# Kernel tuning notes

Measured on AMD Instinct MI355X. Metric: run time of the kernel, lower is better.

## Reference

```python
import jax, jax.numpy as jnp
import numpy as np
import math


def setup_inputs() -> dict:
    key = jax.random.key(0)
    ks = jax.random.split(key, 7)
    d_input, d_state, d_output = 256, 256, 256
    B_, S_ = 8, 4096
    x = jax.random.normal(ks[0], (B_, S_, d_input), dtype=jnp.float32)
    log_lambda_real = jax.random.normal(ks[1], (d_state,), dtype=jnp.float32)
    lambda_imag = jax.random.normal(ks[2], (d_state,), dtype=jnp.float32)
    dt = jnp.clip(0.01 + jax.random.normal(ks[3], (d_state,), dtype=jnp.float32) * 0.01, 0.005, 0.1)
    log_dt = jnp.log(dt)
    B = jax.random.normal(ks[4], (d_state, d_input), dtype=jnp.float32) / d_state ** 0.5
    C_real = jax.random.normal(ks[5], (d_output, d_state), dtype=jnp.float32) / d_state ** 0.5
    C_imag = jax.random.normal(ks[6], (d_output, d_state), dtype=jnp.float32) / d_state ** 0.5
    return {"x": x, "log_lambda_real": log_lambda_real, "lambda_imag": lambda_imag,
            "log_dt": log_dt, "B": B, "C_real": C_real, "C_imag": C_imag}


def reference(x, log_lambda_real, lambda_imag, log_dt, B, C_real, C_imag):
    batch, seq_len, _ = x.shape
    # continuous-time poles and step sizes
    Lambda = -jnp.exp(log_lambda_real) + 1j * lambda_imag            # [N] complex
    dt = jnp.clip(jnp.exp(log_dt), 0.005, 0.1)                       # [N]
    # bilinear discretization
    denom = 1.0 - 0.5 * dt * Lambda                                  # [N] complex
    A_bar = (1.0 + 0.5 * dt * Lambda) / denom                        # [N] complex
    B_bar = (dt / denom)[:, None] * B                                # [N, d_in] complex
    # project input into state space: u[b,s,n] (complex)
    u = jnp.matmul(x, B_bar.real.T) + 1j * jnp.matmul(x, B_bar.imag.T)  # [B,S,N]
    # kernel A^0 .. A^{L-1} via cumprod (faithful to original)
    A_poles = jnp.broadcast_to(A_bar[:, None], (A_bar.shape[0], seq_len))  # [N,S]
    A_cp = jnp.cumprod(A_poles, axis=1)
    A_powers = jnp.concatenate([jnp.ones_like(A_cp[:, :1]), A_cp[:, :-1]], axis=1)  # [N,S]
    # FFT causal convolution
    n_fft = 2 ** math.ceil(math.log2(seq_len * 2 - 1))
    u_t = jnp.swapaxes(u, 1, 2)                                      # [B,N,S]
    u_f = jnp.fft.fft(u_t, n=n_fft, axis=-1)                          # [B,N,F]
    A_f = jnp.fft.fft(A_powers, n=n_fft, axis=-1)                     # [N,F]
    h = jnp.fft.ifft(u_f * A_f[None], n=n_fft, axis=-1)[..., :seq_len]  # [B,N,S]
    h = jnp.swapaxes(h, 1, 2)                                         # [B,S,N]
    # output projection, keep real part
    C_c = C_real + 1j * C_imag                                        # [d_out,N]
    return jnp.matmul(h, C_c.T).real                                  # [B,S,d_out]
```

## Files before the change

kernel.cpp:

```cpp
#include <hip/hip_runtime.h>
#include <hip/hip_bf16.h>

#define BB 8
#define SS 4096
#define NN 256
#define MM (BB*SS)
#define CHUNK 32
#define NCH (SS/CHUNK)

#define WS_FINR_B  ((size_t)0)
#define WS_FINI_B  ((size_t)1  << 20)
#define WS_HLR_B   ((size_t)2  << 20)
#define WS_HLI_B   ((size_t)18 << 20)
#define WS_CP_B    ((size_t)34 << 20)

typedef __bf16 bf16_t;
typedef bf16_t bf16x8 __attribute__((ext_vector_type(8)));
typedef float  f32x4  __attribute__((ext_vector_type(4)));
typedef unsigned int u32x4 __attribute__((ext_vector_type(4)));

__device__ inline bf16_t f2b(float f) {
    __hip_bfloat16 h = __float2bfloat16(f);
    return __builtin_bit_cast(bf16_t, h);
}
__device__ inline float b2f(bf16_t v) {
    unsigned u = (unsigned)__builtin_bit_cast(unsigned short, v) << 16;
    return __builtin_bit_cast(float, u);
}
__device__ inline float b2f_lo(unsigned v) {
    unsigned u = v << 16; return __builtin_bit_cast(float, u);
}
__device__ inline float b2f_hi(unsigned v) {
    unsigned u = v & 0xffff0000u; return __builtin_bit_cast(float, u);
}
__device__ inline unsigned pack2(float lo, float hi) {
    unsigned a = (unsigned)__builtin_bit_cast(unsigned short, f2b(lo));
    unsigned b = (unsigned)__builtin_bit_cast(unsigned short, f2b(hi));
    return a | (b << 16);
}
__device__ inline bf16x8 cvt8(f32x4 a, f32x4 b) {
    bf16x8 o;
    o[0]=f2b(a[0]); o[1]=f2b(a[1]); o[2]=f2b(a[2]); o[3]=f2b(a[3]);
    o[4]=f2b(b[0]); o[5]=f2b(b[1]); o[6]=f2b(b[2]); o[7]=f2b(b[3]);
    return o;
}

__device__ inline void ssm_consts(const float* llr, const float* li, const float* ldt,
                                  int n, float& Ar, float& Ai, float& sr, float& si) {
    float lr = -expf(llr[n]);
    float im = li[n];
    float dt = expf(ldt[n]);
    dt = fminf(fmaxf(dt, 0.005f), 0.1f);
    float hr = 0.5f * dt * lr, hi = 0.5f * dt * im;
    float dr = 1.f - hr, di = -hi;
    float inv = 1.f / (dr*dr + di*di);
    Ar = ((1.f + hr)*dr + hi*di) * inv;
    Ai = (hi*dr - (1.f + hr)*di) * inv;
    sr = dt * dr * inv;
    si = -dt * di * inv;
}

__global__ __launch_bounds__(256, 2) void k1(const float* __restrict__ X,
                                             const float* __restrict__ Bw,
                                             const float* __restrict__ llr,
                                             const float* __restrict__ li,
                                             const float* __restrict__ ldt,
                                             const float* __restrict__ Cr,
                                             const float* __restrict__ Ci,
                                             __hip_bfloat16* __restrict__ HLR,
                                             __hip_bfloat16* __restrict__ HLI,
                                             float* __restrict__ finr,
                                             float* __restrict__ fini,
                                             u32x4* __restrict__ Cpack) {
    __shared__ __align__(16) char smem[65536];
    bf16x8* lds_a = (bf16x8*)smem;
    bf16x8* lds_b = (bf16x8*)(smem + 16384);
    __hip_bfloat16 (*vt)[128]  = (__hip_bfloat16(*)[128])(smem + 32768);
    __hip_bfloat16 (*hit)[128] = (__hip_bfloat16(*)[128])smem;

    int t = threadIdx.x;
    int bid = blockIdx.x;
    if (bid >= 512) {
        int ks = bid - 512;
        const float* src = (ks < 8) ? Cr : Ci;
        float sign = (ks < 8) ? 1.f : -1.f;
        #pragma unroll
        for (int jj = 0; jj < 4; ++jj) {
            int s = t + 256 * jj;
            int ot = s >> 6, lane = s & 63;
            int o  = ot*16 + (lane & 15);
            int kb = (ks & 7)*32 + (lane >> 4)*8;
            bf16x8 v;
            #pragma unroll
            for (int e = 0; e < 8; ++e) v[e] = f2b(sign * src[o*256 + kb + e]);
            Cpack[(ks*16 + ot)*64 + lane] = __builtin_bit_cast(u32x4, v);
        }
        return;
    }

    int w = t >> 6, lane = t & 63;
    int q = lane >> 4, r = lane & 15;
    int Nblk = bid & 1, Mblk = bid >> 1;
    int wmt = (w & 1) * 4;
    int wnt = (w >> 1) * 4;
    f32x4 acc[4][4] = {};

    for (int kk = 0; kk < 4; ++kk) {
        int k0 = kk * 64;
        #pragma unroll
        for (int s = 0; s < 4; ++s) {
            int f    = s * 256 + t;
            int tile = f >> 6;
            int ls   = f & 63;
            int mt   = tile >> 1, kb = tile & 1;
            int qq   = ls >> 4, rr = ls & 15;
            int col  = k0 + kb * 32 + qq * 8;
            const f32x4* pa = (const f32x4*)(X  + (size_t)(Mblk*128 + mt*16 + rr) * 256 + col);
            const f32x4* pb = (const f32x4*)(Bw + (size_t)(Nblk*128 + mt*16 + rr) * 256 + col);
            lds_a[f] = cvt8(pa[0], pa[1]);
            lds_b[f] = cvt8(pb[0], pb[1]);
        }
        __syncthreads();
        #pragma unroll
        for (int kb = 0; kb < 2; ++kb) {
            bf16x8 af[4], bfr[4];
            #pragma unroll
            for (int i = 0; i < 4; ++i) {
                af[i]  = lds_a[((wmt + i)*2 + kb)*64 + lane];
                bfr[i] = lds_b[((wnt + i)*2 + kb)*64 + lane];
            }
            #pragma unroll
            for (int mt = 0; mt < 4; ++mt)
                #pragma unroll
                for (int nt = 0; nt < 4; ++nt)
                    acc[mt][nt] = __builtin_amdgcn_mfma_f32_16x16x32_bf16(
                        af[mt], bfr[nt], acc[mt][nt], 0, 0, 0);
        }
        __syncthreads();
    }
    #pragma unroll
    for (int mt = 0; mt < 4; ++mt)
        #pragma unroll
        for (int nt = 0; nt < 4; ++nt)
            #pragma unroll
            for (int reg = 0; reg < 4; ++reg)
                vt[(wmt+mt)*16 + q*4 + reg][(wnt+nt)*16 + r] =
                    __float2bfloat16(acc[mt][nt][reg]);
    __syncthreads();

    int m0 = Mblk * 128;
    int b = m0 >> 12, cbase = (m0 & 4095) >> 5;
    {
        int p = t & 63, ch = t >> 6;
        int n0 = Nblk*128 + p*2;
        float Ar0,Ai0,sr0,si0, Ar1,Ai1,sr1,si1;
        ssm_consts(llr, li, ldt, n0,   Ar0, Ai0, sr0, si0);
        ssm_consts(llr, li, ldt, n0+1, Ar1, Ai1, sr1, si1);
        float hr0=0.f, hi0=0.f, hr1=0.f, hi1=0.f;
        #pragma unroll 8
        for (int i = 0; i < CHUNK; ++i) {
            int row = ch*32 + i;
            unsigned vv = *(unsigned*)&vt[row][p*2];
            float v0 = b2f_lo(vv), v1 = b2f_hi(vv);
            float t0r = fmaf(Ar0, hr0, fmaf(-Ai0, hi0, sr0 * v0));
            float t0i = fmaf(Ar0, hi0, fmaf( Ai0, hr0, si0 * v0));
            float t1r = fmaf(Ar1, hr1, fmaf(-Ai1, hi1, sr1 * v1));
            float t1i = fmaf(Ar1, hi1, fmaf( Ai1, hr1, si1 * v1));
            hr0=t0r; hi0=t0i; hr1=t1r; hi1=t1i;
            *(unsigned*)&vt[row][p*2]  = pack2(hr0, hr1);
            *(unsigned*)&hit[row][p*2] = pack2(hi0, hi1);
        }
        int f = (b * NCH + cbase + ch) * NN + n0;
        finr[f] = hr0; finr[f+1] = hr1;
        fini[f] = hi0; fini[f+1] = hi1;
    }
    __syncthreads();
    #pragma unroll
    for (int jj = 0; jj < 8; ++jj) {
        int s  = t + 256 * jj;
        int rl = s >> 4, cv = s & 15;
        *(u32x4*)(HLR + (size_t)(m0 + rl) * NN + Nblk*128 + cv*8) = *(const u32x4*)&vt[rl][cv*8];
        *(u32x4*)(HLI + (size_t)(m0 + rl) * NN + Nblk*128 + cv*8) = *(const u32x4*)&hit[rl][cv*8];
    }
}

__global__ __launch_bounds__(512, 4) void k3(const __hip_bfloat16* __restrict__ HLR,
                                             const __hip_bfloat16* __restrict__ HLI,
                                             const float* __restrict__ finr,
                                             const float* __restrict__ fini,
                                             const float* __restrict__ llr,
                                             const float* __restrict__ li,
                                             const float* __restrict__ ldt,
                                             const u32x4* __restrict__ Cpack,
                                             float* __restrict__ out) {
    __shared__ __align__(16) char hlds[65536];
    int t = threadIdx.x;
    int m0 = blockIdx.x * 64;
    int b = m0 >> 12, cbase = (m0 & 4095) >> 5;

    {
        int n = t & 255, d = t >> 8;
        float Ar, Ai, sr_, si_;
        ssm_consts(llr, li, ldt, n, Ar, Ai, sr_, si_);
        float Pr = Ar, Pi = Ai;
        #pragma unroll
        for (int i = 0; i < 5; ++i) { float tt = Pr*Pr - Pi*Pi; Pi = 2.f*Pr*Pi; Pr = tt; }
        float cr = 0.f, ci = 0.f;
        int ce = cbase + d;
        #pragma unroll 4
        for (int j = 0; j < ce; ++j) {
            int f = (b * NCH + j) * NN + n;
            float fr = finr[f], fi = fini[f];
            float tr = fmaf(Pr, cr, fmaf(-Pi, ci, fr));
            float ti = fmaf(Pr, ci, fmaf( Pi, cr, fi));
            cr = tr; ci = ti;
        }
        float gr = Ar*cr - Ai*ci;
        float gi = Ar*ci + Ai*cr;
        int oct = n >> 3, j2 = (n & 7) * 2;
        #pragma unroll 8
        for (int i = 0; i < CHUNK; ++i) {
            int row  = d*32 + i;
            int octp = oct ^ (row & 31);
            int off  = ((row*32 + octp) << 4) + j2;
            *(__hip_bfloat16*)(hlds + off)         = __float2bfloat16(gr);
            *(__hip_bfloat16*)(hlds + 32768 + off) = __float2bfloat16(gi);
            float tg = Ar*gr - Ai*gi;
            gi = fmaf(Ar, gi, Ai*gr);
            gr = tg;
        }
    }
    __syncthreads();
    #pragma unroll
    for (int jj = 0; jj < 4; ++jj) {
        int s = t + 512*jj;
        int row = s >> 5, oct = s & 31;
        int octp = oct ^ (row & 31);
        char* ptr_r = hlds + ((row*32 + octp) << 4);
        char* ptr_i = ptr_r + 32768;
        u32x4 hru = *(const u32x4*)(HLR + (size_t)(m0 + row) * NN + oct*8);
        u32x4 hiu = *(const u32x4*)(HLI + (size_t)(m0 + row) * NN + oct*8);
        bf16x8 hl_r = __builtin_bit_cast(bf16x8, hru);
        bf16x8 hl_i = __builtin_bit_cast(bf16x8, hiu);
        bf16x8 g_r = *(const bf16x8*)ptr_r;
        bf16x8 g_i = *(const bf16x8*)ptr_i;
        bf16x8 o_r, o_i;
        #pragma unroll
        for (int e = 0; e < 8; ++e) {
            o_r[e] = f2b(b2f(hl_r[e]) + b2f(g_r[e]));
            o_i[e] = f2b(b2f(hl_i[e]) + b2f(g_i[e]));
        }
        *(bf16x8*)ptr_r = o_r;
        *(bf16x8*)ptr_i = o_i;
    }
    __syncthreads();
    int w = t >> 6, lane = t & 63, q = lane >> 4, r = lane & 15;
    f32x4 acc[4][2] = {};
    #pragma unroll
    for (int ks = 0; ks < 16; ++ks) {
        int base = (ks < 8) ? 0 : 32768;
        int kin  = ks & 7;
        bf16x8 af[4];
        #pragma unroll
        for (int mt = 0; mt < 4; ++mt) {
            int ml   = mt*16 + r;
            int octp = (kin*4 + q) ^ (ml & 31);
            af[mt] = *(const bf16x8*)(hlds + base + ((ml*32 + octp) << 4));
        }
        #pragma unroll
        for (int u = 0; u < 2; ++u) {
            bf16x8 bf_ = __builtin_bit_cast(bf16x8, Cpack[(ks*16 + w*2 + u)*64 + lane]);
            #pragma unroll
            for (int mt = 0; mt < 4; ++mt)
                acc[mt][u] = __builtin_amdgcn_mfma_f32_16x16x32_bf16(
                    af[mt], bf_, acc[mt][u], 0, 0, 0);
        }
    }
    #pragma unroll
    for (int mt = 0; mt < 4; ++mt)
        #pragma unroll
        for (int u = 0; u < 2; ++u)
            #pragma unroll
            for (int reg = 0; reg < 4; ++reg)
                out[(size_t)(m0 + mt*16 + q*4 + reg) * NN + (w*2 + u)*16 + r] =
                    acc[mt][u][reg];
}

extern "C" void kernel_launch(void* const* d_in, const int* in_sizes, int n_in,
                              void* d_out, int out_size, void* d_ws, size_t ws_size,
                              hipStream_t stream) {
    const float* x   = (const float*)d_in[0];
    const float* llr = (const float*)d_in[1];
    const float* li  = (const float*)d_in[2];
    const float* ldt = (const float*)d_in[3];
    const float* Bw  = (const float*)d_in[4];
    const float* Cr  = (const float*)d_in[5];
    const float* Ci  = (const float*)d_in[6];

    char* wsb = (char*)d_ws;
    float* finr = (float*)(wsb + WS_FINR_B);
    float* fini = (float*)(wsb + WS_FINI_B);
    __hip_bfloat16* HLR = (__hip_bfloat16*)(wsb + WS_HLR_B);
    __hip_bfloat16* HLI = (__hip_bfloat16*)(wsb + WS_HLI_B);
    u32x4* Cpack        = (u32x4*)(wsb + WS_CP_B);

    k1<<<528, 256, 0, stream>>>(x, Bw, llr, li, ldt, Cr, Ci,
                                HLR, HLI, finr, fini, Cpack);
    k3<<<512, 512, 0, stream>>>(HLR, HLI, finr, fini, llr, li, ldt,
                                Cpack, (float*)d_out);
}
```

Before: 134.6 us.

## Restructure SSM pipeline into prep, scan, and fix-up kernels staged through output buffer

```diff
diff --git a/kernel.cpp b/kernel.cpp
--- a/kernel.cpp
+++ b/kernel.cpp
@@ -4,15 +4,13 @@
 #define BB 8
 #define SS 4096
 #define NN 256
-#define MM (BB*SS)
 #define CHUNK 32
 #define NCH (SS/CHUNK)
 
-#define WS_FINR_B  ((size_t)0)
-#define WS_FINI_B  ((size_t)1  << 20)
-#define WS_HLR_B   ((size_t)2  << 20)
-#define WS_HLI_B   ((size_t)18 << 20)
-#define WS_CP_B    ((size_t)34 << 20)
+#define WS_FINR_B ((size_t)0)
+#define WS_FINI_B ((size_t)1 << 20)
+#define WS_CP_B   ((size_t)2 << 20)
+#define WS_BP_B   (((size_t)2 << 20) + (256u << 10))
 
 typedef __bf16 bf16_t;
 typedef bf16_t bf16x8 __attribute__((ext_vector_type(8)));
@@ -22,10 +20,6 @@
 __device__ inline bf16_t f2b(float f) {
     __hip_bfloat16 h = __float2bfloat16(f);
     return __builtin_bit_cast(bf16_t, h);
-}
-__device__ inline float b2f(bf16_t v) {
-    unsigned u = (unsigned)__builtin_bit_cast(unsigned short, v) << 16;
-    return __builtin_bit_cast(float, u);
 }
 __device__ inline float b2f_lo(unsigned v) {
     unsigned u = v << 16; return __builtin_bit_cast(float, u);
@@ -60,230 +54,248 @@
     si = -dt * di * inv;
 }
 
-__global__ __launch_bounds__(256, 2) void k1(const float* __restrict__ X,
-                                             const float* __restrict__ Bw,
-                                             const float* __restrict__ llr,
-                                             const float* __restrict__ li,
-                                             const float* __restrict__ ldt,
+__global__ __launch_bounds__(256) void kprep(const float* __restrict__ Bw,
                                              const float* __restrict__ Cr,
                                              const float* __restrict__ Ci,
-                                             __hip_bfloat16* __restrict__ HLR,
-                                             __hip_bfloat16* __restrict__ HLI,
-                                             float* __restrict__ finr,
-                                             float* __restrict__ fini,
-                                             u32x4* __restrict__ Cpack) {
-    __shared__ __align__(16) char smem[65536];
-    bf16x8* lds_a = (bf16x8*)smem;
-    bf16x8* lds_b = (bf16x8*)(smem + 16384);
-    __hip_bfloat16 (*vt)[128]  = (__hip_bfloat16(*)[128])(smem + 32768);
-    __hip_bfloat16 (*hit)[128] = (__hip_bfloat16(*)[128])smem;
-
+                                             u32x4* __restrict__ Cpack,
+                                             u32x4* __restrict__ Bpack) {
+    int t = threadIdx.x, bid = blockIdx.x;
+    const float* src;
+    float sign;
+    u32x4* dst;
+    int ks;
+    if (bid < 16) { ks = bid;      src = (ks < 8) ? Cr : Ci; sign = (ks < 8) ? 1.f : -1.f; dst = Cpack; }
+    else          { ks = bid - 16; src = Bw;                 sign = 1.f;                   dst = Bpack; }
+    int ksl = ks & 7;
+    #pragma unroll
+    for (int jj = 0; jj < 4; ++jj) {
+        int s = t + 256 * jj;
+        int ot = s >> 6, lane = s & 63;
+        int o  = ot*16 + (lane & 15);
+        int kb = ksl*32 + (lane >> 4)*8;
+        bf16x8 v;
+        #pragma unroll
+        for (int e = 0; e < 8; ++e) v[e] = f2b(sign * src[o*256 + kb + e]);
+        dst[(ks*16 + ot)*64 + lane] = __builtin_bit_cast(u32x4, v);
+    }
+}
+
+
+__global__ __launch_bounds__(256, 2) void kA(
+    const float* __restrict__ X,
+    const float* __restrict__ llr,
+    const float* __restrict__ li,
+    const float* __restrict__ ldt,
+    const u32x4* __restrict__ Bpack,
+    float* __restrict__ finr,
+    float* __restrict__ fini,
+    float* __restrict__ out)
+{
+    __shared__ __align__(16) char hlds[65536];
     int t = threadIdx.x;
     int bid = blockIdx.x;
-    if (bid >= 512) {
-        int ks = bid - 512;
-        const float* src = (ks < 8) ? Cr : Ci;
-        float sign = (ks < 8) ? 1.f : -1.f;
-        #pragma unroll
-        for (int jj = 0; jj < 4; ++jj) {
-            int s = t + 256 * jj;
-            int ot = s >> 6, lane = s & 63;
-            int o  = ot*16 + (lane & 15);
-            int kb = (ks & 7)*32 + (lane >> 4)*8;
-            bf16x8 v;
-            #pragma unroll
-            for (int e = 0; e < 8; ++e) v[e] = f2b(sign * src[o*256 + kb + e]);
-            Cpack[(ks*16 + ot)*64 + lane] = __builtin_bit_cast(u32x4, v);
-        }
-        return;
-    }
-
-    int w = t >> 6, lane = t & 63;
-    int q = lane >> 4, r = lane & 15;
-    int Nblk = bid & 1, Mblk = bid >> 1;
-    int wmt = (w & 1) * 4;
-    int wnt = (w >> 1) * 4;
+    int m0 = bid * 64;
+    int b = bid >> 6;
+    int cbase = (bid & 63) * 2;
+    int w = t >> 6, lane = t & 63, q = lane >> 4, r = lane & 15;
+
     f32x4 acc[4][4] = {};
-
     for (int kk = 0; kk < 4; ++kk) {
-        int k0 = kk * 64;
-        #pragma unroll
-        for (int s = 0; s < 4; ++s) {
-            int f    = s * 256 + t;
-            int tile = f >> 6;
-            int ls   = f & 63;
-            int mt   = tile >> 1, kb = tile & 1;
-            int qq   = ls >> 4, rr = ls & 15;
-            int col  = k0 + kb * 32 + qq * 8;
-            const f32x4* pa = (const f32x4*)(X  + (size_t)(Mblk*128 + mt*16 + rr) * 256 + col);
-            const f32x4* pb = (const f32x4*)(Bw + (size_t)(Nblk*128 + mt*16 + rr) * 256 + col);
-            lds_a[f] = cvt8(pa[0], pa[1]);
-            lds_b[f] = cvt8(pb[0], pb[1]);
+        #pragma unroll
+        for (int ss = 0; ss < 2; ++ss) {
+            int s = t + 256 * ss;
+            int m = s >> 3, kg = s & 7;
+            const f32x4* px = (const f32x4*)(X + (size_t)(m0 + m)*256 + kk*64 + kg*8);
+            *(bf16x8*)(hlds + 32768 + m*128 + ((kg ^ (m & 7)) << 4)) = cvt8(px[0], px[1]);
         }
         __syncthreads();
+        bf16x8 bp[2][4], xf[2][4];
         #pragma unroll
         for (int kb = 0; kb < 2; ++kb) {
-            bf16x8 af[4], bfr[4];
-            #pragma unroll
-            for (int i = 0; i < 4; ++i) {
-                af[i]  = lds_a[((wmt + i)*2 + kb)*64 + lane];
-                bfr[i] = lds_b[((wnt + i)*2 + kb)*64 + lane];
+            #pragma unroll
+            for (int nt = 0; nt < 4; ++nt)
+                bp[kb][nt] = __builtin_bit_cast(bf16x8,
+                    Bpack[((kk*2 + kb)*16 + w*4 + nt)*64 + lane]);
+            #pragma unroll
+            for (int mt = 0; mt < 4; ++mt) {
+                int m = mt*16 + r;
+                xf[kb][mt] = *(const bf16x8*)(hlds + 32768 + m*128 +
+                                              (((kb*4 + q) ^ (m & 7)) << 4));
             }
-            #pragma unroll
-            for (int mt = 0; mt < 4; ++mt)
+        }
+        #pragma unroll
+        for (int kb = 0; kb < 2; ++kb)
+            #pragma unroll
+            for (int nt = 0; nt < 4; ++nt)
                 #pragma unroll
-                for (int nt = 0; nt < 4; ++nt)
-                    acc[mt][nt] = __builtin_amdgcn_mfma_f32_16x16x32_bf16(
-                        af[mt], bfr[nt], acc[mt][nt], 0, 0, 0);
-        }
+                for (int mt = 0; mt < 4; ++mt)
+                    acc[nt][mt] = __builtin_amdgcn_mfma_f32_16x16x32_bf16(
+                        bp[kb][nt], xf[kb][mt], acc[nt][mt], 0, 0, 0);
         __syncthreads();
     }
     #pragma unroll
-    for (int mt = 0; mt < 4; ++mt)
-        #pragma unroll
-        for (int nt = 0; nt < 4; ++nt)
-            #pragma unroll
-            for (int reg = 0; reg < 4; ++reg)
-                vt[(wmt+mt)*16 + q*4 + reg][(wnt+nt)*16 + r] =
-                    __float2bfloat16(acc[mt][nt][reg]);
+    for (int nt = 0; nt < 4; ++nt) {
+        int n0 = w*64 + nt*16 + q*4;
+        #pragma unroll
+        for (int mt = 0; mt < 4; ++mt) {
+            int m = mt*16 + r;
+            uint2 d;
+            d.x = pack2(acc[nt][mt][0], acc[nt][mt][1]);
+            d.y = pack2(acc[nt][mt][2], acc[nt][mt][3]);
+            *(uint2*)(hlds + m*512 + (((n0 >> 3) ^ ((m >> 1) & 31)) << 4) + (n0 & 7)*2) = d;
+        }
+    }
     __syncthreads();
 
-    int m0 = Mblk * 128;
-    int b = m0 >> 12, cbase = (m0 & 4095) >> 5;
     {
-        int p = t & 63, ch = t >> 6;
-        int n0 = Nblk*128 + p*2;
+        int p = t & 127, ch = t >> 7;
+        int cb = cbase + ch;
         float Ar0,Ai0,sr0,si0, Ar1,Ai1,sr1,si1;
-        ssm_consts(llr, li, ldt, n0,   Ar0, Ai0, sr0, si0);
-        ssm_consts(llr, li, ldt, n0+1, Ar1, Ai1, sr1, si1);
+        ssm_consts(llr, li, ldt, 2*p,   Ar0, Ai0, sr0, si0);
+        ssm_consts(llr, li, ldt, 2*p+1, Ar1, Ai1, sr1, si1);
         float hr0=0.f, hi0=0.f, hr1=0.f, hi1=0.f;
-        #pragma unroll 8
-        for (int i = 0; i < CHUNK; ++i) {
-            int row = ch*32 + i;
-            unsigned vv = *(unsigned*)&vt[row][p*2];
-            float v0 = b2f_lo(vv), v1 = b2f_hi(vv);
-            float t0r = fmaf(Ar0, hr0, fmaf(-Ai0, hi0, sr0 * v0));
-            float t0i = fmaf(Ar0, hi0, fmaf( Ai0, hr0, si0 * v0));
-            float t1r = fmaf(Ar1, hr1, fmaf(-Ai1, hi1, sr1 * v1));
-            float t1i = fmaf(Ar1, hi1, fmaf( Ai1, hr1, si1 * v1));
+        #pragma unroll
+        for (int i2 = 0; i2 < 16; ++i2) {
+            int row = ch*32 + i2*2;
+            char* a = hlds + row*512 + (((p >> 2) ^ ((row >> 1) & 31)) << 4) + (p & 3)*4;
+            unsigned v0 = *(unsigned*)a;
+            unsigned v1 = *(unsigned*)(a + 512);
+            float x0 = b2f_lo(v0), x1 = b2f_hi(v0);
+            float t0r = fmaf(Ar0, hr0, fmaf(-Ai0, hi0, sr0*x0));
+            float t0i = fmaf(Ar0, hi0, fmaf( Ai0, hr0, si0*x0));
+            float t1r = fmaf(Ar1, hr1, fmaf(-Ai1, hi1, sr1*x1));
+            float t1i = fmaf(Ar1, hi1, fmaf( Ai1, hr1, si1*x1));
             hr0=t0r; hi0=t0i; hr1=t1r; hi1=t1i;
-            *(unsigned*)&vt[row][p*2]  = pack2(hr0, hr1);
-            *(unsigned*)&hit[row][p*2] = pack2(hi0, hi1);
-        }
-        int f = (b * NCH + cbase + ch) * NN + n0;
-        finr[f] = hr0; finr[f+1] = hr1;
-        fini[f] = hi0; fini[f+1] = hi1;
+            *(unsigned*)a           = pack2(hr0, hr1);
+            *(unsigned*)(a + 32768) = pack2(hi0, hi1);
+            x0 = b2f_lo(v1); x1 = b2f_hi(v1);
+            t0r = fmaf(Ar0, hr0, fmaf(-Ai0, hi0, sr0*x0));
+            t0i = fmaf(Ar0, hi0, fmaf( Ai0, hr0, si0*x0));
+            t1r = fmaf(Ar1, hr1, fmaf(-Ai1, hi1, sr1*x1));
+            t1i = fmaf(Ar1, hi1, fmaf( Ai1, hr1, si1*x1));
+            hr0=t0r; hi0=t0i; hr1=t1r; hi1=t1i;
+            *(unsigned*)(a + 512)         = pack2(hr0, hr1);
+            *(unsigned*)(a + 32768 + 512) = pack2(hi0, hi1);
+        }
+        int f0 = (b*NCH + cb)*NN + 2*p;
+        finr[f0] = hr0; finr[f0+1] = hr1;
+        fini[f0] = hi0; fini[f0+1] = hi1;
     }
     __syncthreads();
-    #pragma unroll
-    for (int jj = 0; jj < 8; ++jj) {
-        int s  = t + 256 * jj;
-        int rl = s >> 4, cv = s & 15;
-        *(u32x4*)(HLR + (size_t)(m0 + rl) * NN + Nblk*128 + cv*8) = *(const u32x4*)&vt[rl][cv*8];
-        *(u32x4*)(HLI + (size_t)(m0 + rl) * NN + Nblk*128 + cv*8) = *(const u32x4*)&hit[rl][cv*8];
-    }
-}
-
-__global__ __launch_bounds__(512, 4) void k3(const __hip_bfloat16* __restrict__ HLR,
-                                             const __hip_bfloat16* __restrict__ HLI,
-                                             const float* __restrict__ finr,
-                                             const float* __restrict__ fini,
-                                             const float* __restrict__ llr,
-                                             const float* __restrict__ li,
-                                             const float* __restrict__ ldt,
-                                             const u32x4* __restrict__ Cpack,
-                                             float* __restrict__ out) {
+
+    char* dst = (char*)out + ((size_t)bid << 16);
+    #pragma unroll
+    for (int jj = 0; jj < 16; ++jj)
+        *(u32x4*)(dst + jj*4096 + t*16) = *(const u32x4*)(hlds + jj*4096 + t*16);
+}
+
+__global__ __launch_bounds__(256, 2) void kB(
+    const float* __restrict__ llr,
+    const float* __restrict__ li,
+    const float* __restrict__ ldt,
+    const u32x4* __restrict__ Cpack,
+    const float* __restrict__ finr,
+    const float* __restrict__ fini,
+    float* __restrict__ out)
+{
     __shared__ __align__(16) char hlds[65536];
     int t = threadIdx.x;
-    int m0 = blockIdx.x * 64;
-    int b = m0 >> 12, cbase = (m0 & 4095) >> 5;
-
-    {
-        int n = t & 255, d = t >> 8;
-        float Ar, Ai, sr_, si_;
-        ssm_consts(llr, li, ldt, n, Ar, Ai, sr_, si_);
-        float Pr = Ar, Pi = Ai;
-        #pragma unroll
-        for (int i = 0; i < 5; ++i) { float tt = Pr*Pr - Pi*Pi; Pi = 2.f*Pr*Pi; Pr = tt; }
-        float cr = 0.f, ci = 0.f;
-        int ce = cbase + d;
+    int bid = blockIdx.x;
+    int m0 = bid * 64;
+    int b = bid >> 6;
+    int cbase = (bid & 63) * 2;
+    int w = t >> 6, lane = t & 63, q = lane >> 4, r = lane & 15;
+
+    const char* src = (const char*)out + ((size_t)bid << 16);
+    u32x4 img[16];
+    #pragma unroll
+    for (int jj = 0; jj < 16; ++jj)
+        img[jj] = *(const u32x4*)(src + jj*4096 + t*16);
+
+    int p = t & 127, ch = t >> 7;
+    int cb = cbase + ch;
+    float Ar0,Ai0,sr0,si0, Ar1,Ai1,sr1,si1;
+    ssm_consts(llr, li, ldt, 2*p,   Ar0, Ai0, sr0, si0);
+    ssm_consts(llr, li, ldt, 2*p+1, Ar1, Ai1, sr1, si1);
+    float g0r=0.f, g0i=0.f, g1r=0.f, g1i=0.f;
+    if (cb > 0) {
+        float P0r=Ar0, P0i=Ai0, P1r=Ar1, P1i=Ai1;
+        #pragma unroll
+        for (int i = 0; i < 5; ++i) {
+            float u0 = P0r*P0r - P0i*P0i; P0i = 2.f*P0r*P0i; P0r = u0;
+            float u1 = P1r*P1r - P1i*P1i; P1i = 2.f*P1r*P1i; P1r = u1;
+        }
+        float c0r=0.f, c0i=0.f, c1r=0.f, c1i=0.f;
         #pragma unroll 4
-        for (int j = 0; j < ce; ++j) {
-            int f = (b * NCH + j) * NN + n;
-            float fr = finr[f], fi = fini[f];
-            float tr = fmaf(Pr, cr, fmaf(-Pi, ci, fr));
-            float ti = fmaf(Pr, ci, fmaf( Pi, cr, fi));
-            cr = tr; ci = ti;
-        }
-        float gr = Ar*cr - Ai*ci;
-        float gi = Ar*ci + Ai*cr;
-        int oct = n >> 3, j2 = (n & 7) * 2;
-        #pragma unroll 8
-        for (int i = 0; i < CHUNK; ++i) {
-            int row  = d*32 + i;
-            int octp = oct ^ (row & 31);
-            int off  = ((row*32 + octp) << 4) + j2;
-            *(__hip_bfloat16*)(hlds + off)         = __float2bfloat16(gr);
-            *(__hip_bfloat16*)(hlds + 32768 + off) = __float2bfloat16(gi);
-            float tg = Ar*gr - Ai*gi;
-            gi = fmaf(Ar, gi, Ai*gr);
-            gr = tg;
-        }
-    }
+        for (int j = 0; j < cb; ++j) {
+            int ff = (b*NCH + j)*NN + 2*p;
+            float2 fr = *(const float2*)(finr + ff);
+            float2 fi = *(const float2*)(fini + ff);
+            float n0r = fmaf(P0r, c0r, fmaf(-P0i, c0i, fr.x));
+            float n0i = fmaf(P0r, c0i, fmaf( P0i, c0r, fi.x));
+            float n1r = fmaf(P1r, c1r, fmaf(-P1i, c1i, fr.y));
+            float n1i = fmaf(P1r, c1i, fmaf( P1i, c1r, fi.y));
+            c0r=n0r; c0i=n0i; c1r=n1r; c1i=n1i;
+        }
+        g0r = Ar0*c0r - Ai0*c0i; g0i = Ar0*c0i + Ai0*c0r;
+        g1r = Ar1*c1r - Ai1*c1i; g1i = Ar1*c1i + Ai1*c1r;
+    }
+
+    #pragma unroll
+    for (int jj = 0; jj < 16; ++jj)
+        *(u32x4*)(hlds + jj*4096 + t*16) = img[jj];
     __syncthreads();
-    #pragma unroll
-    for (int jj = 0; jj < 4; ++jj) {
-        int s = t + 512*jj;
-        int row = s >> 5, oct = s & 31;
-        int octp = oct ^ (row & 31);
-        char* ptr_r = hlds + ((row*32 + octp) << 4);
-        char* ptr_i = ptr_r + 32768;
-        u32x4 hru = *(const u32x4*)(HLR + (size_t)(m0 + row) * NN + oct*8);
-        u32x4 hiu = *(const u32x4*)(HLI + (size_t)(m0 + row) * NN + oct*8);
-        bf16x8 hl_r = __builtin_bit_cast(bf16x8, hru);
-        bf16x8 hl_i = __builtin_bit_cast(bf16x8, hiu);
-        bf16x8 g_r = *(const bf16x8*)ptr_r;
-        bf16x8 g_i = *(const bf16x8*)ptr_i;
-        bf16x8 o_r, o_i;
-        #pragma unroll
-        for (int e = 0; e < 8; ++e) {
-            o_r[e] = f2b(b2f(hl_r[e]) + b2f(g_r[e]));
-            o_i[e] = f2b(b2f(hl_i[e]) + b2f(g_i[e]));
-        }
-        *(bf16x8*)ptr_r = o_r;
-        *(bf16x8*)ptr_i = o_i;
+
+    if (cb > 0) {
+        #pragma unroll
+        for (int i2 = 0; i2 < 16; ++i2) {
+            int row = ch*32 + i2*2;
+            char* a = hlds + row*512 + (((p >> 2) ^ ((row >> 1) & 31)) << 4) + (p & 3)*4;
+            unsigned ur0 = *(unsigned*)a;
+            unsigned ur1 = *(unsigned*)(a + 512);
+            unsigned ui0 = *(unsigned*)(a + 32768);
+            unsigned ui1 = *(unsigned*)(a + 32768 + 512);
+            *(unsigned*)a           = pack2(b2f_lo(ur0) + g0r, b2f_hi(ur0) + g1r);
+            *(unsigned*)(a + 32768) = pack2(b2f_lo(ui0) + g0i, b2f_hi(ui0) + g1i);
+            { float t0 = Ar0*g0r - Ai0*g0i; g0i = fmaf(Ar0, g0i, Ai0*g0r); g0r = t0;
+              float t1 = Ar1*g1r - Ai1*g1i; g1i = fmaf(Ar1, g1i, Ai1*g1r); g1r = t1; }
+            *(unsigned*)(a + 512)         = pack2(b2f_lo(ur1) + g0r, b2f_hi(ur1) + g1r);
+            *(unsigned*)(a + 32768 + 512) = pack2(b2f_lo(ui1) + g0i, b2f_hi(ui1) + g1i);
+            { float t0 = Ar0*g0r - Ai0*g0i; g0i = fmaf(Ar0, g0i, Ai0*g0r); g0r = t0;
+              float t1 = Ar1*g1r - Ai1*g1i; g1i = fmaf(Ar1, g1i, Ai1*g1r); g1r = t1; }
+        }
     }
     __syncthreads();
-    int w = t >> 6, lane = t & 63, q = lane >> 4, r = lane & 15;
-    f32x4 acc[4][2] = {};
+
+    f32x4 acc2[4][4] = {};
     #pragma unroll
     for (int ks = 0; ks < 16; ++ks) {
-        int base = (ks < 8) ? 0 : 32768;
-        int kin  = ks & 7;
+        int base = (ks & 8) ? 32768 : 0;
+        int kin = ks & 7;
         bf16x8 af[4];
         #pragma unroll
         for (int mt = 0; mt < 4; ++mt) {
-            int ml   = mt*16 + r;
-            int octp = (kin*4 + q) ^ (ml & 31);
-            af[mt] = *(const bf16x8*)(hlds + base + ((ml*32 + octp) << 4));
-        }
-        #pragma unroll
-        for (int u = 0; u < 2; ++u) {
-            bf16x8 bf_ = __builtin_bit_cast(bf16x8, Cpack[(ks*16 + w*2 + u)*64 + lane]);
+            int row = mt*16 + r;
+            af[mt] = *(const bf16x8*)(hlds + base + row*512 +
+                     (((kin*4 + q) ^ ((row >> 1) & 31)) << 4));
+        }
+        #pragma unroll
+        for (int nt = 0; nt < 4; ++nt) {
+            bf16x8 cf = __builtin_bit_cast(bf16x8, Cpack[(ks*16 + w*4 + nt)*64 + lane]);
             #pragma unroll
             for (int mt = 0; mt < 4; ++mt)
-                acc[mt][u] = __builtin_amdgcn_mfma_f32_16x16x32_bf16(
-                    af[mt], bf_, acc[mt][u], 0, 0, 0);
+                acc2[mt][nt] = __builtin_amdgcn_mfma_f32_16x16x32_bf16(
+                    af[mt], cf, acc2[mt][nt], 0, 0, 0);
         }
     }
     #pragma unroll
     for (int mt = 0; mt < 4; ++mt)
         #pragma unroll
-        for (int u = 0; u < 2; ++u)
+        for (int nt = 0; nt < 4; ++nt)
             #pragma unroll
             for (int reg = 0; reg < 4; ++reg)
-                out[(size_t)(m0 + mt*16 + q*4 + reg) * NN + (w*2 + u)*16 + r] =
-                    acc[mt][u][reg];
+                out[(size_t)(m0 + mt*16 + q*4 + reg)*NN + w*64 + nt*16 + r] =
+                    acc2[mt][nt][reg];
 }
 
 extern "C" void kernel_launch(void* const* d_in, const int* in_sizes, int n_in,
@@ -298,14 +310,13 @@
     const float* Ci  = (const float*)d_in[6];
 
     char* wsb = (char*)d_ws;
-    float* finr = (float*)(wsb + WS_FINR_B);
-    float* fini = (float*)(wsb + WS_FINI_B);
-    __hip_bfloat16* HLR = (__hip_bfloat16*)(wsb + WS_HLR_B);
-    __hip_bfloat16* HLI = (__hip_bfloat16*)(wsb + WS_HLI_B);
-    u32x4* Cpack        = (u32x4*)(wsb + WS_CP_B);
-
-    k1<<<528, 256, 0, stream>>>(x, Bw, llr, li, ldt, Cr, Ci,
-                                HLR, HLI, finr, fini, Cpack);
-    k3<<<512, 512, 0, stream>>>(HLR, HLI, finr, fini, llr, li, ldt,
-                                Cpack, (float*)d_out);
-}
+    float* finr  = (float*)(wsb + WS_FINR_B);
+    float* fini  = (float*)(wsb + WS_FINI_B);
+    u32x4* Cpack = (u32x4*)(wsb + WS_CP_B);
+    u32x4* Bpack = (u32x4*)(wsb + WS_BP_B);
+    float* outp  = (float*)d_out;
+
+    kprep<<<24, 256, 0, stream>>>(Bw, Cr, Ci, Cpack, Bpack);
+    kA<<<512, 256, 0, stream>>>(x, llr, li, ldt, Bpack, finr, fini, outp);
+    kB<<<512, 256, 0, stream>>>(llr, li, ldt, Cpack, finr, fini, outp);
+}
```

Result: faster. 131.7 us (-2.2%).
